# Optimization experiments

Measured on AMD Instinct MI355X. Metric: run time of the kernel, lower is better.

## Reference

```python
import math
import jax, jax.numpy as jnp
import numpy as np

D_MODEL = 1024
L_MAX = 4096
BATCH = 2
FILTER_ORDER = 64
EMB_DIM = 3


def _make_z(L, emb_dim=EMB_DIM):
    # PositionalEmbedding: [time, real bands, imag bands] -> [1, L, emb_dim]
    t = jnp.linspace(0.0, 1.0, L)[None, :, None]
    bands = (emb_dim - 1) // 2
    t_res = jnp.linspace(0.0, L - 1.0, L)[None, :, None]
    w = 2.0 * math.pi * t_res / L
    f = jnp.linspace(1e-4, float(bands - 1), bands)[None, None]
    ph = f * w  # z = exp(-1j*ph) -> real=cos(ph), imag=-sin(ph)
    return jnp.concatenate([t, jnp.cos(ph), -jnp.sin(ph)], axis=-1).astype(jnp.float32)


def setup_inputs() -> dict:
    key = jax.random.key(0)
    ks = jax.random.split(key, 16)
    d = D_MODEL
    iw = 3 * d  # inner_width = d_model * (order + 1), order=2

    def rn(k, shape, scale):
        return (jax.random.normal(k, shape) * scale).astype(jnp.float32)

    return {
        'u': rn(ks[0], (BATCH, L_MAX, d), 1.0),
        'w_in': rn(ks[1], (iw, d), d ** -0.5),
        'b_in': rn(ks[2], (iw,), 0.01),
        'sf_w': rn(ks[3], (iw, 1, 3), 3 ** -0.5),
        'sf_b': rn(ks[4], (iw,), 0.01),
        'z': _make_z(L_MAX),
        'w0': rn(ks[5], (FILTER_ORDER, EMB_DIM), EMB_DIM ** -0.5),
        'b0': rn(ks[6], (FILTER_ORDER,), 0.01),
        'freq': jnp.ones((1, FILTER_ORDER), dtype=jnp.float32),  # Sin(w=1)
        'w1': rn(ks[7], (FILTER_ORDER, FILTER_ORDER), FILTER_ORDER ** -0.5),
        'b1': rn(ks[8], (FILTER_ORDER,), 0.01),
        'w2': rn(ks[9], (FILTER_ORDER, FILTER_ORDER), FILTER_ORDER ** -0.5),
        'b2': rn(ks[10], (FILTER_ORDER,), 0.01),
        'wf': rn(ks[11], (d, FILTER_ORDER), FILTER_ORDER ** -0.5),
        'D': rn(ks[12], (d,), 1.0),
        'w_out': rn(ks[13], (d, d), d ** -0.5),
        'b_out': rn(ks[14], (d,), 0.01),
    }


def _dwconv(x, w, b):
    # depthwise Conv1d(kernel=3, padding=2, groups=C); x: [B, C, L] -> [B, C, L+2]
    y = jax.lax.conv_general_dilated(
        x, w, window_strides=(1,), padding=[(2, 2)],
        feature_group_count=x.shape[1],
        dimension_numbers=('NCH', 'OIH', 'NCH'))
    return y + b[None, :, None]


def _fftconv(v, k, D):
    # circular conv via zero-padded FFT; torch's k_f/fft_size with norm='forward'
    # irfft cancels to the standard (norm='backward') inverse.
    L = v.shape[-1]
    n = 2 * L
    y = jnp.fft.irfft(jnp.fft.rfft(v, n=n) * jnp.fft.rfft(k, n=n), n=n)[..., :L]
    return y + v * D[:, None]


def reference(u, w_in, b_in, sf_w, sf_b, z, w0, b0, freq, w1, b1, w2, b2, wf, D, w_out, b_out):
    b, l, d = u.shape
    L = min(l, L_MAX)

    # input projection + short depthwise filter
    up = jnp.einsum('bld,ed->ble', u, w_in) + b_in  # [b, l, 3d]
    up = up.transpose(0, 2, 1)                       # [b, 3d, l]
    uc = _dwconv(up, sf_w, sf_b)[..., :L]            # [b, 3d, L]
    x0, x1, v = jnp.split(uc, 3, axis=1)             # each [b, d, L]

    # implicit filter MLP with shared Sin activation
    h = jnp.sin(freq * (z @ w0.T + b0))              # [1, L, 64]
    h = jnp.sin(freq * (h @ w1.T + b1))
    h = jnp.sin(freq * (h @ w2.T + b2))
    h = h @ wf.T                                     # [1, L, d]

    # exponential modulation (buffers: t, deltas)
    t = jnp.linspace(0.0, 1.0, L)[None, :, None]
    max_decay = math.log(0.01) / 0.3
    min_decay = math.log(0.01) / 1.5
    deltas = jnp.linspace(min_decay, max_decay, d)[None, None]
    h = h * jnp.exp(-t * jnp.abs(deltas))            # [1, L, d]
    k = h[0].T                                       # [d, L]

    # hyena recurrence (order=2 -> one gated fft conv)
    v = _fftconv(v * x1, k, D)
    y = (v * x0).transpose(0, 2, 1)                  # [b, L, d]
    return jnp.einsum('bld,ed->ble', y, w_out) + b_out
```

## Files before the change

kernel.cpp:

```cpp
#include <hip/hip_runtime.h>
#include <math.h>

#define DM   1024
#define LL   4096
#define NB   2
#define E3   3072
#define FPI  3.14159265358979323846f

typedef __bf16 bf16x8 __attribute__((ext_vector_type(8)));
typedef float  f32x4  __attribute__((ext_vector_type(4)));
typedef _Float16 f16x2 __attribute__((ext_vector_type(2)));

__device__ __forceinline__ unsigned short f2bf(float x) {
    unsigned u = __float_as_uint(x);
    u += 0x7fffu + ((u >> 16) & 1u);
    return (unsigned short)(u >> 16);
}
__device__ __forceinline__ void gload16(void* lds, const void* g) {
    typedef const __attribute__((address_space(1))) unsigned int* gp_t;
    typedef __attribute__((address_space(3))) unsigned int* lp_t;
    __builtin_amdgcn_global_load_lds((gp_t)g, (lp_t)lds, 16, 0, 0);
}

__global__ __launch_bounds__(256) void k_cvt_bf16(
    const float* __restrict__ in, ushort* __restrict__ out, int n4)
{
    int idx = blockIdx.x * 256 + threadIdx.x;
    int stride = gridDim.x * 256;
    for (int i = idx; i < n4; i += stride) {
        float4 v = reinterpret_cast<const float4*>(in)[i];
        ushort4 o;
        o.x = f2bf(v.x); o.y = f2bf(v.y); o.z = f2bf(v.z); o.w = f2bf(v.w);
        *reinterpret_cast<ushort4*>(out + 4 * i) = o;
    }
}

__global__ __launch_bounds__(512, 2) void k_gemm256(
    const ushort* __restrict__ A, const ushort* __restrict__ B,
    const float* __restrict__ bias, float* __restrict__ C,
    int Ntiles, int ldc)
{
    __shared__ __align__(16) char ldsm[131072];
    const int tid  = threadIdx.x;
    const int lane = tid & 63;
    const int w    = tid >> 6;
    const int wr   = w >> 2, wc = w & 3;

    const int cpx = gridDim.x >> 3;
    int swz = (blockIdx.x & 7) * cpx + (blockIdx.x >> 3);
    const int m0 = (swz / Ntiles) << 8;
    const int n0 = (swz % Ntiles) << 8;

    const int r0 = tid >> 2;
    const int swzc = ((tid & 3) ^ ((r0 >> 1) & 3)) << 4;
    const char* Asrc = (const char*)A + ((size_t)(m0 + r0) << 11) + swzc;
    const char* Bsrc = (const char*)B + ((size_t)(n0 + r0) << 11) + swzc;
    char* Ld = ldsm + tid * 16;

    const int lm = lane & 15, lk = lane >> 4;
    const int rA = wr * 128 + lm;
    const int rB = wc * 64 + lm;
    const int aBase = rA * 64 + ((lk ^ ((rA >> 1) & 3)) << 4);
    const int bBase = 32768 + rB * 64 + ((lk ^ ((rB >> 1) & 3)) << 4);

#define STG_A(ks, nb, t1) do { \
    gload16(Ld + (nb) + (ks)*16384,        Asrc + (t1)*128 + (ks)*64); \
    gload16(Ld + (nb) + (ks)*16384 + 8192, Asrc + (t1)*128 + (ks)*64 + 262144); } while(0)
#define STG_B(ks, nb, t1) do { \
    gload16(Ld + (nb) + 32768 + (ks)*16384,        Bsrc + (t1)*128 + (ks)*64); \
    gload16(Ld + (nb) + 32768 + (ks)*16384 + 8192, Bsrc + (t1)*128 + (ks)*64 + 262144); } while(0)
#define LDA(buf, ks, m) (*(const bf16x8*)(ldsm + (buf) + (ks)*16384 + aBase + (m)*1024))
#define LDB(buf, ks, n) (*(const bf16x8*)(ldsm + (buf) + (ks)*16384 + bBase + (n)*1024))
#define VMCNT4() asm volatile("s_waitcnt vmcnt(4)" ::: "memory")
#define VMCNT0() asm volatile("s_waitcnt vmcnt(0)" ::: "memory")
#define BAR() __builtin_amdgcn_s_barrier()

    f32x4 acc[8][4];
#pragma unroll
    for (int i = 0; i < 8; ++i)
#pragma unroll
        for (int j = 0; j < 4; ++j)
#pragma unroll
            for (int r = 0; r < 4; ++r) acc[i][j][r] = 0.f;

    STG_A(0, 0, 0); STG_B(0, 0, 0); STG_A(1, 0, 0); STG_B(1, 0, 0);
    VMCNT4();
    BAR();

    bf16x8 af[4], bq[4];
#pragma unroll 1
    for (int t = 0; t < 15; ++t) {
        const int buf = (t & 1) << 16;
        const int nb  = ((t + 1) & 1) << 16;
        const int t1  = t + 1;
#pragma unroll
        for (int n = 0; n < 4; ++n) bq[n] = LDB(buf, 0, n);
#pragma unroll
        for (int m = 0; m < 4; ++m) af[m] = LDA(buf, 0, m);
        STG_A(0, nb, t1);
        BAR();
        __builtin_amdgcn_s_setprio(1);
#pragma unroll
        for (int m = 0; m < 4; ++m)
#pragma unroll
            for (int n = 0; n < 4; ++n)
                acc[m][n] = __builtin_amdgcn_mfma_f32_16x16x32_bf16(af[m], bq[n], acc[m][n], 0, 0, 0);
        __builtin_amdgcn_s_setprio(0);
        BAR();
#pragma unroll
        for (int m = 0; m < 4; ++m) af[m] = LDA(buf, 0, 4 + m);
        STG_B(0, nb, t1);
        VMCNT4();
        BAR();
        __builtin_amdgcn_s_setprio(1);
#pragma unroll
        for (int m = 0; m < 4; ++m)
#pragma unroll
            for (int n = 0; n < 4; ++n)
                acc[4 + m][n] = __builtin_amdgcn_mfma_f32_16x16x32_bf16(af[m], bq[n], acc[4 + m][n], 0, 0, 0);
        __builtin_amdgcn_s_setprio(0);
        BAR();
#pragma unroll
        for (int n = 0; n < 4; ++n) bq[n] = LDB(buf, 1, n);
#pragma unroll
        for (int m = 0; m < 4; ++m) af[m] = LDA(buf, 1, m);
        STG_A(1, nb, t1);
        BAR();
        __builtin_amdgcn_s_setprio(1);
#pragma unroll
        for (int m = 0; m < 4; ++m)
#pragma unroll
            for (int n = 0; n < 4; ++n)
                acc[m][n] = __builtin_amdgcn_mfma_f32_16x16x32_bf16(af[m], bq[n], acc[m][n], 0, 0, 0);
        __builtin_amdgcn_s_setprio(0);
        BAR();
#pragma unroll
        for (int m = 0; m < 4; ++m) af[m] = LDA(buf, 1, 4 + m);
        STG_B(1, nb, t1);
        VMCNT4();
        BAR();
        __builtin_amdgcn_s_setprio(1);
#pragma unroll
        for (int m = 0; m < 4; ++m)
#pragma unroll
            for (int n = 0; n < 4; ++n)
                acc[4 + m][n] = __builtin_amdgcn_mfma_f32_16x16x32_bf16(af[m], bq[n], acc[4 + m][n], 0, 0, 0);
        __builtin_amdgcn_s_setprio(0);
        BAR();
    }
    {
        const int buf = 1 << 16;
#pragma unroll
        for (int n = 0; n < 4; ++n) bq[n] = LDB(buf, 0, n);
#pragma unroll
        for (int m = 0; m < 4; ++m) af[m] = LDA(buf, 0, m);
        BAR();
#pragma unroll
        for (int m = 0; m < 4; ++m)
#pragma unroll
            for (int n = 0; n < 4; ++n)
                acc[m][n] = __builtin_amdgcn_mfma_f32_16x16x32_bf16(af[m], bq[n], acc[m][n], 0, 0, 0);
        BAR();
#pragma unroll
        for (int m = 0; m < 4; ++m) af[m] = LDA(buf, 0, 4 + m);
        VMCNT0();
        BAR();
#pragma unroll
        for (int m = 0; m < 4; ++m)
#pragma unroll
            for (int n = 0; n < 4; ++n)
                acc[4 + m][n] = __builtin_amdgcn_mfma_f32_16x16x32_bf16(af[m], bq[n], acc[4 + m][n], 0, 0, 0);
        BAR();
#pragma unroll
        for (int n = 0; n < 4; ++n) bq[n] = LDB(buf, 1, n);
#pragma unroll
        for (int m = 0; m < 4; ++m) af[m] = LDA(buf, 1, m);
        BAR();
#pragma unroll
        for (int m = 0; m < 4; ++m)
#pragma unroll
            for (int n = 0; n < 4; ++n)
                acc[m][n] = __builtin_amdgcn_mfma_f32_16x16x32_bf16(af[m], bq[n], acc[m][n], 0, 0, 0);
        BAR();
#pragma unroll
        for (int m = 0; m < 4; ++m) af[m] = LDA(buf, 1, 4 + m);
        BAR();
#pragma unroll
        for (int m = 0; m < 4; ++m)
#pragma unroll
            for (int n = 0; n < 4; ++n)
                acc[4 + m][n] = __builtin_amdgcn_mfma_f32_16x16x32_bf16(af[m], bq[n], acc[4 + m][n], 0, 0, 0);
    }
    const int er = lk << 2, ec = lm;
#pragma unroll
    for (int m = 0; m < 8; ++m) {
        int row = m0 + wr * 128 + m * 16 + er;
#pragma unroll
        for (int n = 0; n < 4; ++n) {
            int col = n0 + wc * 64 + n * 16 + ec;
            float bz = bias[col];
            float* cp = C + (size_t)row * ldc + col;
#pragma unroll
            for (int r = 0; r < 4; ++r)
                cp[(size_t)r * ldc] = acc[m][n][r] + bz;
        }
    }
#undef STG_A
#undef STG_B
#undef LDA
#undef LDB
#undef VMCNT4
#undef VMCNT0
#undef BAR
}

__global__ __launch_bounds__(256) void k_gemm_bf16(
    const ushort* __restrict__ A, const ushort* __restrict__ B,
    const float* __restrict__ bias, float* __restrict__ C, int ldc)
{
    __shared__ ushort As[128 * 32];
    __shared__ ushort Bs[128 * 32];
    const int tid  = threadIdx.x;
    const int lane = tid & 63;
    const int w    = tid >> 6;
    const int wm   = (w >> 1) << 6, wn = (w & 1) << 6;
    const int m0   = blockIdx.y << 7, n0 = blockIdx.x << 7;

    f32x4 acc[4][4];
#pragma unroll
    for (int i = 0; i < 4; ++i)
#pragma unroll
        for (int j = 0; j < 4; ++j)
#pragma unroll
            for (int r = 0; r < 4; ++r) acc[i][j][r] = 0.f;

    const char* Ab = (const char*)A + ((size_t)(m0 + (tid >> 2)) << 11) + ((tid & 3) << 4);
    const char* Bb = (const char*)B + ((size_t)(n0 + (tid >> 2)) << 11) + ((tid & 3) << 4);
    char* AsD = (char*)As + tid * 16;
    char* BsD = (char*)Bs + tid * 16;
    const char* ap = (const char*)As + ((wm + (lane & 15)) << 6) + ((lane >> 4) << 4);
    const char* bp = (const char*)Bs + ((wn + (lane & 15)) << 6) + ((lane >> 4) << 4);

    for (int k0 = 0; k0 < 1024; k0 += 32) {
        __syncthreads();
        gload16(AsD,        Ab + k0 * 2);
        gload16(AsD + 4096, Ab + 131072 + k0 * 2);
        gload16(BsD,        Bb + k0 * 2);
        gload16(BsD + 4096, Bb + 131072 + k0 * 2);
        __syncthreads();
        bf16x8 af[4], bfr[4];
#pragma unroll
        for (int i = 0; i < 4; ++i) {
            af[i]  = *(const bf16x8*)(ap + (i << 10));
            bfr[i] = *(const bf16x8*)(bp + (i << 10));
        }
#pragma unroll
        for (int i = 0; i < 4; ++i)
#pragma unroll
            for (int j = 0; j < 4; ++j)
                acc[i][j] = __builtin_amdgcn_mfma_f32_16x16x32_bf16(
                    af[i], bfr[j], acc[i][j], 0, 0, 0);
    }
    const int er = (lane >> 4) << 2;
    const int ec = lane & 15;
#pragma unroll
    for (int i = 0; i < 4; ++i) {
        int row = m0 + wm + (i << 4) + er;
#pragma unroll
        for (int j = 0; j < 4; ++j) {
            int col = n0 + wn + (j << 4) + ec;
            float bz = bias[col];
            float* cp = C + (size_t)row * ldc + col;
#pragma unroll
            for (int r = 0; r < 4; ++r)
                cp[(size_t)r * ldc] = acc[i][j][r] + bz;
        }
    }
}

__global__ __launch_bounds__(256) void k_dwconv(
    const float* __restrict__ up, const float* __restrict__ sfw,
    const float* __restrict__ sfb, float* __restrict__ x0t,
    float* __restrict__ vin)
{
    __shared__ float xT[32][65];
    __shared__ float vT[32][65];
    const int b  = blockIdx.z;
    const int t0 = blockIdx.y * 64;
    const int c0 = blockIdx.x * 32;
    const int tid = threadIdx.x;
    const int cL = tid & 31, tL = tid >> 5;
    const float* upb = up + (size_t)b * LL * E3;
    const int c = c0 + cL;

#pragma unroll
    for (int r = 0; r < 8; ++r) {
        int t_local = (r << 3) + tL;
        int t = t0 + t_local;
        float res[3];
#pragma unroll
        for (int s3 = 0; s3 < 3; ++s3) {
            int e = c + (s3 << 10);
            float w0 = sfw[e*3+0], w1 = sfw[e*3+1], w2 = sfw[e*3+2];
            float xa = (t >= 2) ? upb[(size_t)(t-2)*E3 + e] : 0.f;
            float xb = (t >= 1) ? upb[(size_t)(t-1)*E3 + e] : 0.f;
            float xc = upb[(size_t)t*E3 + e];
            res[s3] = w0*xa + w1*xb + w2*xc + sfb[e];
        }
        xT[cL][t_local] = res[0];
        vT[cL][t_local] = res[1] * res[2];
    }
    __syncthreads();
    const int cW = tid >> 3, q = tid & 7;
    float tmp[8];
#pragma unroll
    for (int i = 0; i < 8; ++i) tmp[i] = xT[cW][8*q + i];
    size_t off = ((size_t)b * DM + c0 + cW) * LL + t0 + 8*q;
    *reinterpret_cast<float4*>(x0t + off)     = make_float4(tmp[0], tmp[1], tmp[2], tmp[3]);
    *reinterpret_cast<float4*>(x0t + off + 4) = make_float4(tmp[4], tmp[5], tmp[6], tmp[7]);
#pragma unroll
    for (int i = 0; i < 8; ++i) tmp[i] = vT[cW][8*q + i];
    *reinterpret_cast<float4*>(vin + off)     = make_float4(tmp[0], tmp[1], tmp[2], tmp[3]);
    *reinterpret_cast<float4*>(vin + off + 4) = make_float4(tmp[4], tmp[5], tmp[6], tmp[7]);
}

__global__ __launch_bounds__(256) void k_filt_mlp(
    const float* __restrict__ z, const float* __restrict__ w0,
    const float* __restrict__ b0, const float* __restrict__ fr,
    const float* __restrict__ w1, const float* __restrict__ b1,
    const float* __restrict__ w2, const float* __restrict__ b2,
    float* __restrict__ H3)
{
    __shared__ float w1t[64 * 65];
    __shared__ float w2t[64 * 65];
    __shared__ float hb[4][64];
    const int tid = threadIdx.x;
    for (int idx = tid; idx < 4096; idx += 256) {
        int j = idx >> 6, m = idx & 63;
        w1t[m*65 + j] = w1[idx];
        w2t[m*65 + j] = w2[idx];
    }
    __syncthreads();
    const int tl = tid >> 6, j = tid & 63;
    const float frj = fr[j];
    const float b0j = b0[j], b1j = b1[j], b2j = b2[j];
    const float w00 = w0[j*3+0], w01 = w0[j*3+1], w02 = w0[j*3+2];
    const int t0 = blockIdx.x * 64;
    for (int r = 0; r < 16; ++r) {
        int t = t0 + r*4 + tl;
        float z0 = z[t*3+0], z1 = z[t*3+1], z2 = z[t*3+2];
        float h = sinf(frj * (b0j + z0*w00 + z1*w01 + z2*w02));
        hb[tl][j] = h;
        __syncthreads();
        float s = b1j;
#pragma unroll
        for (int m = 0; m < 64; ++m) s = fmaf(hb[tl][m], w1t[m*65 + j], s);
        __syncthreads();
        h = sinf(frj * s);
        hb[tl][j] = h;
        __syncthreads();
        s = b2j;
#pragma unroll
        for (int m = 0; m < 64; ++m) s = fmaf(hb[tl][m], w2t[m*65 + j], s);
        h = sinf(frj * s);
        H3[(size_t)t * 64 + j] = h;
        __syncthreads();
    }
}

__global__ __launch_bounds__(256) void k_filt_k(
    const float* __restrict__ H3, const float* __restrict__ wf,
    float* __restrict__ kf)
{
    __shared__ float Hs[64][65];
    __shared__ float Ws[64][65];
    const int tid = threadIdx.x;
    const int t0 = blockIdx.x * 64, d0 = blockIdx.y * 64;
    for (int idx = tid; idx < 4096; idx += 256) {
        int r = idx >> 6, cc = idx & 63;
        Hs[r][cc] = H3[(size_t)(t0 + r) * 64 + cc];
        Ws[r][cc] = wf[(size_t)(d0 + r) * 64 + cc];
    }
    __syncthreads();
    const int tx = tid & 15, ty = tid >> 4;
    float acc[4][4];
#pragma unroll
    for (int i = 0; i < 4; ++i)
#pragma unroll
        for (int jj = 0; jj < 4; ++jj) acc[i][jj] = 0.f;
#pragma unroll
    for (int j = 0; j < 64; ++j) {
        float wv[4], hv[4];
#pragma unroll
        for (int i = 0; i < 4; ++i) wv[i] = Ws[4*ty + i][j];
#pragma unroll
        for (int i = 0; i < 4; ++i) hv[i] = Hs[4*tx + i][j];
#pragma unroll
        for (int i = 0; i < 4; ++i)
#pragma unroll
            for (int jj = 0; jj < 4; ++jj) acc[i][jj] = fmaf(wv[i], hv[jj], acc[i][jj]);
    }
    const float mind = -3.0701134573253944f;
    const float maxd = -15.350567286626972f;
#pragma unroll
    for (int i = 0; i < 4; ++i) {
        int d = d0 + 4*ty + i;
        float delta = fabsf(mind + (maxd - mind) * ((float)d / 1023.f));
#pragma unroll
        for (int jj = 0; jj < 4; ++jj) {
            int t = t0 + 4*tx + jj;
            float tn = (float)t / 4095.f;
            kf[(size_t)d * LL + t] = acc[i][jj] * expf(-tn * delta);
        }
    }
}

__device__ __forceinline__ int pidx(int p) { return p + (p >> 4); }

__device__ __forceinline__ float2 cmul(float2 a, float2 b) {
    return make_float2(a.x*b.x - a.y*b.y, a.x*b.y + a.y*b.x);
}

__device__ void fft_lds_fwd4(float2* buf, int tid) {
    int lh = 10;
#pragma unroll
    for (int h = 2048; h >= 32; h >>= 2, lh -= 2) {
        const int hh = h >> 1;
        const float rinv = -FPI / (float)h;
        __syncthreads();
#pragma unroll
        for (int r = 0; r < 4; ++r) {
            int bf = (r << 9) + tid;
            int q  = bf & (hh - 1);
            int g  = bf >> lh;
            int j  = (g << (lh + 2)) + q;
            float2 a = buf[pidx(j)];
            float2 b = buf[pidx(j + hh)];
            float2 c = buf[pidx(j + h)];
            float2 d = buf[pidx(j + h + hh)];
            float2 t0 = make_float2(a.x + c.x, a.y + c.y);
            float2 t1 = make_float2(a.x - c.x, a.y - c.y);
            float2 t2 = make_float2(b.x + d.x, b.y + d.y);
            float2 t3 = make_float2(b.y - d.y, d.x - b.x);
            float sn, cs;
            __sincosf(rinv * (float)q, &sn, &cs);
            float c2 = cs*cs - sn*sn, s2 = 2.f*cs*sn;
            float c3 = cs*c2 - sn*s2, s3 = cs*s2 + sn*c2;
            buf[pidx(j)] = make_float2(t0.x + t2.x, t0.y + t2.y);
            float2 e1 = make_float2(t0.x - t2.x, t0.y - t2.y);
            buf[pidx(j + hh)] = make_float2(e1.x*c2 - e1.y*s2, e1.x*s2 + e1.y*c2);
            float2 e2 = make_float2(t1.x + t3.x, t1.y + t3.y);
            buf[pidx(j + h)] = make_float2(e2.x*cs - e2.y*sn, e2.x*sn + e2.y*cs);
            float2 e3 = make_float2(t1.x - t3.x, t1.y - t3.y);
            buf[pidx(j + h + hh)] = make_float2(e3.x*c3 - e3.y*s3, e3.x*s3 + e3.y*c3);
        }
    }
    __syncthreads();
}

__device__ void fft_lds_inv4(float2* buf, int tid) {
    int lh = 4;
#pragma unroll
    for (int h = 32; h <= 2048; h <<= 2, lh += 2) {
        const int hh = h >> 1;
        const float rpos = FPI / (float)h;
        __syncthreads();
#pragma unroll
        for (int r = 0; r < 4; ++r) {
            int bf = (r << 9) + tid;
            int q  = bf & (hh - 1);
            int g  = bf >> lh;
            int j  = (g << (lh + 2)) + q;
            float2 o0 = buf[pidx(j)];
            float2 o1 = buf[pidx(j + hh)];
            float2 o2 = buf[pidx(j + h)];
            float2 o3 = buf[pidx(j + h + hh)];
            float sn, cs;
            __sincosf(rpos * (float)q, &sn, &cs);
            float c2 = cs*cs - sn*sn, s2 = 2.f*cs*sn;
            float c3 = cs*c2 - sn*s2, s3 = cs*s2 + sn*c2;
            float2 p1 = make_float2(o1.x*c2 - o1.y*s2, o1.x*s2 + o1.y*c2);
            float2 p2 = make_float2(o2.x*cs - o2.y*sn, o2.x*sn + o2.y*cs);
            float2 p3 = make_float2(o3.x*c3 - o3.y*s3, o3.x*s3 + o3.y*c3);
            float2 u0 = make_float2(o0.x + p1.x, o0.y + p1.y);
            float2 u1 = make_float2(o0.x - p1.x, o0.y - p1.y);
            float2 u2 = make_float2(p2.x + p3.x, p2.y + p3.y);
            float2 u3 = make_float2(p2.x - p3.x, p2.y - p3.y);
            float2 ib = make_float2(-u3.y, u3.x);
            buf[pidx(j)]          = make_float2(u0.x + u2.x, u0.y + u2.y);
            buf[pidx(j + hh)]     = make_float2(u1.x + ib.x, u1.y + ib.y);
            buf[pidx(j + h)]      = make_float2(u0.x - u2.x, u0.y - u2.y);
            buf[pidx(j + h + hh)] = make_float2(u1.x - ib.x, u1.y - ib.y);
        }
    }
    __syncthreads();
}

__device__ __forceinline__ void fft_reg_fwd(float2* c) {
    const float W16r[8] = {1.f, 0.92387953f, 0.70710678f, 0.38268343f,
                           0.f, -0.38268343f, -0.70710678f, -0.92387953f};
    const float W16i[8] = {0.f, -0.38268343f, -0.70710678f, -0.92387953f,
                           -1.f, -0.92387953f, -0.70710678f, -0.38268343f};
#pragma unroll
    for (int k = 0; k < 8; ++k) {
        float2 a = c[k], b = c[k+8];
        float2 d = make_float2(a.x - b.x, a.y - b.y);
        c[k]   = make_float2(a.x + b.x, a.y + b.y);
        c[k+8] = cmul(d, make_float2(W16r[k], W16i[k]));
    }
    const float W8r[4] = {1.f, 0.70710678f, 0.f, -0.70710678f};
    const float W8i[4] = {0.f, -0.70710678f, -1.f, -0.70710678f};
#pragma unroll
    for (int blk = 0; blk < 16; blk += 8)
#pragma unroll
        for (int k = 0; k < 4; ++k) {
            float2 a = c[blk+k], b = c[blk+k+4];
            float2 d = make_float2(a.x - b.x, a.y - b.y);
            c[blk+k]   = make_float2(a.x + b.x, a.y + b.y);
            c[blk+k+4] = cmul(d, make_float2(W8r[k], W8i[k]));
        }
#pragma unroll
    for (int blk = 0; blk < 16; blk += 4) {
        {   float2 a = c[blk], b = c[blk+2];
            c[blk]   = make_float2(a.x + b.x, a.y + b.y);
            c[blk+2] = make_float2(a.x - b.x, a.y - b.y); }
        {   float2 a = c[blk+1], b = c[blk+3];
            float2 d = make_float2(a.x - b.x, a.y - b.y);
            c[blk+1] = make_float2(a.x + b.x, a.y + b.y);
            c[blk+3] = make_float2(d.y, -d.x); }
    }
#pragma unroll
    for (int blk = 0; blk < 16; blk += 2) {
        float2 a = c[blk], b = c[blk+1];
        c[blk]   = make_float2(a.x + b.x, a.y + b.y);
        c[blk+1] = make_float2(a.x - b.x, a.y - b.y);
    }
}

__device__ __forceinline__ void fft_reg_inv(float2* c) {
#pragma unroll
    for (int blk = 0; blk < 16; blk += 2) {
        float2 a = c[blk], b = c[blk+1];
        c[blk]   = make_float2(a.x + b.x, a.y + b.y);
        c[blk+1] = make_float2(a.x - b.x, a.y - b.y);
    }
#pragma unroll
    for (int blk = 0; blk < 16; blk += 4) {
        {   float2 a = c[blk], b = c[blk+2];
            c[blk]   = make_float2(a.x + b.x, a.y + b.y);
            c[blk+2] = make_float2(a.x - b.x, a.y - b.y); }
        {   float2 a = c[blk+1], b = c[blk+3];
            float2 bt = make_float2(-c[blk+3].y, c[blk+3].x);
            c[blk+1] = make_float2(a.x + bt.x, a.y + bt.y);
            c[blk+3] = make_float2(a.x - bt.x, a.y - bt.y); }
    }
    const float W8r[4] = {1.f, 0.70710678f, 0.f, -0.70710678f};
    const float W8i[4] = {0.f, 0.70710678f, 1.f, 0.70710678f};
#pragma unroll
    for (int blk = 0; blk < 16; blk += 8)
#pragma unroll
        for (int k = 0; k < 4; ++k) {
            float2 a = c[blk+k], b = c[blk+k+4];
            float2 bt = cmul(b, make_float2(W8r[k], W8i[k]));
            c[blk+k]   = make_float2(a.x + bt.x, a.y + bt.y);
            c[blk+k+4] = make_float2(a.x - bt.x, a.y - bt.y);
        }
    const float W16r[8] = {1.f, 0.92387953f, 0.70710678f, 0.38268343f,
                           0.f, -0.38268343f, -0.70710678f, -0.92387953f};
    const float W16i[8] = {0.f, 0.38268343f, 0.70710678f, 0.92387953f,
                           1.f, 0.92387953f, 0.70710678f, 0.38268343f};
#pragma unroll
    for (int k = 0; k < 8; ++k) {
        float2 a = c[k], b = c[k+8];
        float2 bt = cmul(b, make_float2(W16r[k], W16i[k]));
        c[k]   = make_float2(a.x + bt.x, a.y + bt.y);
        c[k+8] = make_float2(a.x - bt.x, a.y - bt.y);
    }
}

__global__ __launch_bounds__(512) void k_kfft(
    const float* __restrict__ kf, f16x2* __restrict__ Kf)
{
    __shared__ float2 buf[8704];
    const int d = blockIdx.x, tid = threadIdx.x;
    const float* krow = kf + (size_t)d * LL;
    const float rinv0 = -FPI / 4096.f;
    for (int i = tid; i < 1024; i += 512) {
        float4 k4 = reinterpret_cast<const float4*>(krow)[i];
        int p = 4 * i;
        float kv[4] = {k4.x, k4.y, k4.z, k4.w};
#pragma unroll
        for (int q = 0; q < 4; ++q) {
            float sn, cs;
            __sincosf(rinv0 * (float)(p + q), &sn, &cs);
            buf[pidx(p + q)]        = make_float2(kv[q], 0.f);
            buf[pidx(p + q + 4096)] = make_float2(kv[q] * cs, kv[q] * sn);
        }
    }
    fft_lds_fwd4(buf, tid);
    float2 c[16];
    const int p0 = tid * 16;
#pragma unroll
    for (int j = 0; j < 16; ++j) c[j] = buf[pidx(p0 + j)];
    fft_reg_fwd(c);
    f16x2* outp = Kf + (size_t)d * 8192 + p0;
#pragma unroll
    for (int j = 0; j < 16; ++j) {
        f16x2 o;
        o[0] = (_Float16)(c[j].x * (1.f/8192.f));
        o[1] = (_Float16)(c[j].y * (1.f/8192.f));
        outp[j] = o;
    }
}

__global__ __launch_bounds__(512) void k_fftconv(
    const float* __restrict__ vin, const f16x2* __restrict__ Kf,
    const float* __restrict__ x0t, const float* __restrict__ Dp,
    ushort* __restrict__ yg)
{
    __shared__ float2 buf[8704];
    const int d = blockIdx.x, tid = threadIdx.x;
    const float* vrow0 = vin + (size_t)d * LL;
    const float* vrow1 = vin + ((size_t)DM + d) * LL;
    const float rinv0 = -FPI / 4096.f;
    for (int i = tid; i < 1024; i += 512) {
        float4 a4 = reinterpret_cast<const float4*>(vrow0)[i];
        float4 b4 = reinterpret_cast<const float4*>(vrow1)[i];
        int p = 4 * i;
        float ar[4] = {a4.x, a4.y, a4.z, a4.w};
        float br[4] = {b4.x, b4.y, b4.z, b4.w};
#pragma unroll
        for (int q = 0; q < 4; ++q) {
            float sn, cs;
            __sincosf(rinv0 * (float)(p + q), &sn, &cs);
            float2 z = make_float2(ar[q], br[q]);
            buf[pidx(p + q)]        = z;
            buf[pidx(p + q + 4096)] = cmul(z, make_float2(cs, sn));
        }
    }
    fft_lds_fwd4(buf, tid);
    float2 c[16];
    const int p0 = tid * 16;
#pragma unroll
    for (int j = 0; j < 16; ++j) c[j] = buf[pidx(p0 + j)];
    fft_reg_fwd(c);
    const f16x2* kfr = Kf + (size_t)d * 8192 + p0;
#pragma unroll
    for (int j = 0; j < 16; ++j) {
        f16x2 kv = kfr[j];
        c[j] = cmul(c[j], make_float2((float)kv[0], (float)kv[1]));
    }
    fft_reg_inv(c);
#pragma unroll
    for (int j = 0; j < 16; ++j) buf[pidx(p0 + j)] = c[j];
    fft_lds_inv4(buf, tid);
    const float Dd = Dp[d];
    const float* xrow0 = x0t + (size_t)d * LL;
    const float* xrow1 = x0t + ((size_t)DM + d) * LL;
    ushort* orow0 = yg + (size_t)d * LL;
    ushort* orow1 = yg + ((size_t)DM + d) * LL;
    const float rinv4 = FPI / 4096.f;
    for (int i = tid; i < 1024; i += 512) {
        float4 v0 = reinterpret_cast<const float4*>(vrow0)[i];
        float4 v1 = reinterpret_cast<const float4*>(vrow1)[i];
        float4 x0 = reinterpret_cast<const float4*>(xrow0)[i];
        float4 x1 = reinterpret_cast<const float4*>(xrow1)[i];
        int p = 4 * i;
        float vr0[4] = {v0.x, v0.y, v0.z, v0.w};
        float vr1[4] = {v1.x, v1.y, v1.z, v1.w};
        float xr0[4] = {x0.x, x0.y, x0.z, x0.w};
        float xr1[4] = {x1.x, x1.y, x1.z, x1.w};
        ushort s0[4], s1[4];
#pragma unroll
        for (int q = 0; q < 4; ++q) {
            float sn, cs;
            __sincosf(rinv4 * (float)(p + q), &sn, &cs);
            float2 a  = buf[pidx(p + q)];
            float2 bb = buf[pidx(p + q + 4096)];
            float2 bt = cmul(bb, make_float2(cs, sn));
            float yre = a.x + bt.x;
            float yim = a.y + bt.y;
            s0[q] = f2bf((yre + Dd * vr0[q]) * xr0[q]);
            s1[q] = f2bf((yim + Dd * vr1[q]) * xr1[q]);
        }
        *reinterpret_cast<ushort4*>(orow0 + p) = make_ushort4(s0[0], s0[1], s0[2], s0[3]);
        *reinterpret_cast<ushort4*>(orow1 + p) = make_ushort4(s1[0], s1[1], s1[2], s1[3]);
    }
}

__global__ __launch_bounds__(256) void k_tr(
    const ushort* __restrict__ yg, ushort* __restrict__ Ag)
{
    __shared__ ushort S[64][72];
    const int b  = blockIdx.z;
    const int d0 = blockIdx.y * 64;
    const int t0 = blockIdx.x * 64;
    const int tid = threadIdx.x;
#pragma unroll
    for (int p = 0; p < 2; ++p) {
        int idx = p * 256 + tid;
        int dr = idx >> 3, c8 = (idx & 7) << 3;
        uint4 v = *reinterpret_cast<const uint4*>(
            yg + ((size_t)b * DM + d0 + dr) * LL + t0 + c8);
        *reinterpret_cast<uint4*>(&S[dr][c8]) = v;
    }
    __syncthreads();
#pragma unroll
    for (int p = 0; p < 2; ++p) {
        int idx = p * 256 + tid;
        int tr = idx >> 3, dq = (idx & 7) << 3;
        ushort tmp[8] __attribute__((aligned(16)));
#pragma unroll
        for (int q = 0; q < 8; ++q) tmp[q] = S[dq + q][tr];
        *reinterpret_cast<uint4*>(Ag + ((size_t)b * LL + t0 + tr) * DM + d0 + dq) =
            *reinterpret_cast<uint4*>(tmp);
    }
}

extern "C" void kernel_launch(void* const* d_in, const int* in_sizes, int n_in,
                              void* d_out, int out_size, void* d_ws, size_t ws_size,
                              hipStream_t stream)
{
    if (n_in < 17) return;
    const float* u    = (const float*)d_in[0];
    const float* w_in = (const float*)d_in[1];
    const float* b_in = (const float*)d_in[2];
    const float* sf_w = (const float*)d_in[3];
    const float* sf_b = (const float*)d_in[4];
    const float* z    = (const float*)d_in[5];
    const float* w0   = (const float*)d_in[6];
    const float* b0   = (const float*)d_in[7];
    const float* freq = (const float*)d_in[8];
    const float* w1   = (const float*)d_in[9];
    const float* b1   = (const float*)d_in[10];
    const float* w2   = (const float*)d_in[11];
    const float* b2   = (const float*)d_in[12];
    const float* wf   = (const float*)d_in[13];
    const float* Dp   = (const float*)d_in[14];
    const float* wout = (const float*)d_in[15];
    const float* bout = (const float*)d_in[16];
    float* out = (float*)d_out;
    float* ws  = (float*)d_ws;

    float*  up    = ws;
    f16x2*  Kf    = (f16x2*)ws;
    float*  kfbuf = ws + 16777216;
    ushort* yg    = (ushort*)(ws + 16777216);
    float*  H3    = ws + 20971520;
    ushort* Ag    = (ushort*)(ws + 20971520);
    ushort* ub    = (ushort*)(ws + 25165824);
    float*  x0t   = ws + 25165824;
    ushort* wb    = (ushort*)(ws + 33554432);
    float*  vin   = ws + 33554432;
    ushort* woutb = (ushort*)(ws + 33554432);
    const size_t NEED = (size_t)41943040 * 4;
    if (ws_size < NEED) return;

    hipLaunchKernelGGL(k_cvt_bf16, dim3(2048), dim3(256), 0, stream, u, ub, 2097152);
    hipLaunchKernelGGL(k_cvt_bf16, dim3(2048), dim3(256), 0, stream, w_in, wb, 786432);
    hipLaunchKernelGGL(k_gemm256, dim3((8192/256) * (E3/256)), dim3(512), 0, stream,
                       ub, wb, b_in, up, E3/256, E3);
    hipLaunchKernelGGL(k_dwconv,   dim3(DM/32, LL/64, NB), dim3(256), 0, stream,
                       up, sf_w, sf_b, x0t, vin);
    hipLaunchKernelGGL(k_filt_mlp, dim3(LL/64), dim3(256), 0, stream,
                       z, w0, b0, freq, w1, b1, w2, b2, H3);
    hipLaunchKernelGGL(k_filt_k,   dim3(LL/64, DM/64), dim3(256), 0, stream,
                       H3, wf, kfbuf);
    hipLaunchKernelGGL(k_kfft,     dim3(DM), dim3(512), 0, stream,
                       kfbuf, Kf);
    hipLaunchKernelGGL(k_fftconv,  dim3(DM), dim3(512), 0, stream,
                       vin, Kf, x0t, Dp, yg);
    hipLaunchKernelGGL(k_cvt_bf16, dim3(1024), dim3(256), 0, stream, wout, woutb, 262144);
    hipLaunchKernelGGL(k_tr,       dim3(LL/64, DM/64, NB), dim3(256), 0, stream,
                       yg, Ag);
    hipLaunchKernelGGL(k_gemm_bf16, dim3(DM/128, 8192/128), dim3(256), 0, stream,
                       Ag, woutb, bout, out, DM);
}
```

Before: 267.5 us.

## Store input projection in bf16, merge conversions, unroll FFT stages, recur twiddles

The input-projection GEMM now writes bf16 instead of fp32, and the depthwise conv widens those values back to float. This halves the traffic on the large intermediate. The two bf16 conversion kernels are merged into one launch. The radix-4 FFT stages are fully unrolled so each stage computes its twiddle once per thread. The pre/post twiddles switch from per-element sincos to a rotation recurrence. The price is bf16 rounding of the projection output and some accumulated twiddle error across four recurrence steps.

```diff
diff --git a/kernel.cpp b/kernel.cpp
--- a/kernel.cpp
+++ b/kernel.cpp
@@ -16,10 +16,31 @@
     u += 0x7fffu + ((u >> 16) & 1u);
     return (unsigned short)(u >> 16);
 }
+__device__ __forceinline__ float bf2f(ushort s) {
+    return __uint_as_float(((unsigned)s) << 16);
+}
 __device__ __forceinline__ void gload16(void* lds, const void* g) {
     typedef const __attribute__((address_space(1))) unsigned int* gp_t;
     typedef __attribute__((address_space(3))) unsigned int* lp_t;
     __builtin_amdgcn_global_load_lds((gp_t)g, (lp_t)lds, 16, 0, 0);
+}
+
+__global__ __launch_bounds__(256) void k_cvt2(
+    const float* __restrict__ a, ushort* __restrict__ oa, int n4a,
+    const float* __restrict__ b, ushort* __restrict__ ob, int n4b)
+{
+    int idx = blockIdx.x * 256 + threadIdx.x;
+    int stride = gridDim.x * 256;
+    int tot = n4a + n4b;
+    for (int i = idx; i < tot; i += stride) {
+        const float4* src; ushort* dst; int k;
+        if (i < n4a) { src = (const float4*)a; dst = oa; k = i; }
+        else         { src = (const float4*)b; dst = ob; k = i - n4a; }
+        float4 v = src[k];
+        ushort4 o;
+        o.x = f2bf(v.x); o.y = f2bf(v.y); o.z = f2bf(v.z); o.w = f2bf(v.w);
+        *reinterpret_cast<ushort4*>(dst + 4 * k) = o;
+    }
 }
 
 __global__ __launch_bounds__(256) void k_cvt_bf16(
@@ -37,7 +58,7 @@
 
 __global__ __launch_bounds__(512, 2) void k_gemm256(
     const ushort* __restrict__ A, const ushort* __restrict__ B,
-    const float* __restrict__ bias, float* __restrict__ C,
+    const float* __restrict__ bias, ushort* __restrict__ C,
     int Ntiles, int ldc)
 {
     __shared__ __align__(16) char ldsm[131072];
@@ -199,10 +220,10 @@
         for (int n = 0; n < 4; ++n) {
             int col = n0 + wc * 64 + n * 16 + ec;
             float bz = bias[col];
-            float* cp = C + (size_t)row * ldc + col;
+            ushort* cp = C + (size_t)row * ldc + col;
 #pragma unroll
             for (int r = 0; r < 4; ++r)
-                cp[(size_t)r * ldc] = acc[m][n][r] + bz;
+                cp[(size_t)r * ldc] = f2bf(acc[m][n][r] + bz);
         }
     }
 #undef STG_A
@@ -279,7 +300,7 @@
 }
 
 __global__ __launch_bounds__(256) void k_dwconv(
-    const float* __restrict__ up, const float* __restrict__ sfw,
+    const ushort* __restrict__ up, const float* __restrict__ sfw,
     const float* __restrict__ sfb, float* __restrict__ x0t,
     float* __restrict__ vin)
 {
@@ -290,7 +311,7 @@
     const int c0 = blockIdx.x * 32;
     const int tid = threadIdx.x;
     const int cL = tid & 31, tL = tid >> 5;
-    const float* upb = up + (size_t)b * LL * E3;
+    const ushort* upb = up + (size_t)b * LL * E3;
     const int c = c0 + cL;
 
 #pragma unroll
@@ -302,9 +323,9 @@
         for (int s3 = 0; s3 < 3; ++s3) {
             int e = c + (s3 << 10);
             float w0 = sfw[e*3+0], w1 = sfw[e*3+1], w2 = sfw[e*3+2];
-            float xa = (t >= 2) ? upb[(size_t)(t-2)*E3 + e] : 0.f;
-            float xb = (t >= 1) ? upb[(size_t)(t-1)*E3 + e] : 0.f;
-            float xc = upb[(size_t)t*E3 + e];
+            float xa = (t >= 2) ? bf2f(upb[(size_t)(t-2)*E3 + e]) : 0.f;
+            float xb = (t >= 1) ? bf2f(upb[(size_t)(t-1)*E3 + e]) : 0.f;
+            float xc = bf2f(upb[(size_t)t*E3 + e]);
             res[s3] = w0*xa + w1*xb + w2*xc + sfb[e];
         }
         xT[cL][t_local] = res[0];
@@ -421,77 +442,153 @@
     return make_float2(a.x*b.x - a.y*b.y, a.x*b.y + a.y*b.x);
 }
 
+__device__ __forceinline__ void r4f_bfly(float2* buf, int j, int hh,
+    float cs, float sn, float c2, float s2, float c3, float s3)
+{
+    float2 a = buf[pidx(j)];
+    float2 b = buf[pidx(j + hh)];
+    float2 c = buf[pidx(j + 2*hh)];
+    float2 d = buf[pidx(j + 3*hh)];
+    float2 t0 = make_float2(a.x + c.x, a.y + c.y);
+    float2 t1 = make_float2(a.x - c.x, a.y - c.y);
+    float2 t2 = make_float2(b.x + d.x, b.y + d.y);
+    float2 t3 = make_float2(b.y - d.y, d.x - b.x);
+    buf[pidx(j)] = make_float2(t0.x + t2.x, t0.y + t2.y);
+    float2 e1 = make_float2(t0.x - t2.x, t0.y - t2.y);
+    buf[pidx(j + hh)]   = make_float2(e1.x*c2 - e1.y*s2, e1.x*s2 + e1.y*c2);
+    float2 e2 = make_float2(t1.x + t3.x, t1.y + t3.y);
+    buf[pidx(j + 2*hh)] = make_float2(e2.x*cs - e2.y*sn, e2.x*sn + e2.y*cs);
+    float2 e3 = make_float2(t1.x - t3.x, t1.y - t3.y);
+    buf[pidx(j + 3*hh)] = make_float2(e3.x*c3 - e3.y*s3, e3.x*s3 + e3.y*c3);
+}
+
+__device__ __forceinline__ void r4i_bfly(float2* buf, int j, int hh,
+    float cs, float sn, float c2, float s2, float c3, float s3)
+{
+    float2 o0 = buf[pidx(j)];
+    float2 o1 = buf[pidx(j + hh)];
+    float2 o2 = buf[pidx(j + 2*hh)];
+    float2 o3 = buf[pidx(j + 3*hh)];
+    float2 p1 = make_float2(o1.x*c2 - o1.y*s2, o1.x*s2 + o1.y*c2);
+    float2 p2 = make_float2(o2.x*cs - o2.y*sn, o2.x*sn + o2.y*cs);
+    float2 p3 = make_float2(o3.x*c3 - o3.y*s3, o3.x*s3 + o3.y*c3);
+    float2 u0 = make_float2(o0.x + p1.x, o0.y + p1.y);
+    float2 u1 = make_float2(o0.x - p1.x, o0.y - p1.y);
+    float2 u2 = make_float2(p2.x + p3.x, p2.y + p3.y);
+    float2 u3 = make_float2(p2.x - p3.x, p2.y - p3.y);
+    float2 ib = make_float2(-u3.y, u3.x);
+    buf[pidx(j)]        = make_float2(u0.x + u2.x, u0.y + u2.y);
+    buf[pidx(j + hh)]   = make_float2(u1.x + ib.x, u1.y + ib.y);
+    buf[pidx(j + 2*hh)] = make_float2(u0.x - u2.x, u0.y - u2.y);
+    buf[pidx(j + 3*hh)] = make_float2(u1.x - ib.x, u1.y - ib.y);
+}
+
+#define TWCHAIN(cs, sn, c2, s2, c3, s3) \
+    float c2 = cs*cs - sn*sn, s2 = 2.f*cs*sn; \
+    float c3 = cs*c2 - sn*s2, s3 = cs*s2 + sn*c2
+
 __device__ void fft_lds_fwd4(float2* buf, int tid) {
-    int lh = 10;
-#pragma unroll
-    for (int h = 2048; h >= 32; h >>= 2, lh -= 2) {
-        const int hh = h >> 1;
-        const float rinv = -FPI / (float)h;
-        __syncthreads();
-#pragma unroll
-        for (int r = 0; r < 4; ++r) {
-            int bf = (r << 9) + tid;
-            int q  = bf & (hh - 1);
-            int g  = bf >> lh;
-            int j  = (g << (lh + 2)) + q;
-            float2 a = buf[pidx(j)];
-            float2 b = buf[pidx(j + hh)];
-            float2 c = buf[pidx(j + h)];
-            float2 d = buf[pidx(j + h + hh)];
-            float2 t0 = make_float2(a.x + c.x, a.y + c.y);
-            float2 t1 = make_float2(a.x - c.x, a.y - c.y);
-            float2 t2 = make_float2(b.x + d.x, b.y + d.y);
-            float2 t3 = make_float2(b.y - d.y, d.x - b.x);
-            float sn, cs;
-            __sincosf(rinv * (float)q, &sn, &cs);
-            float c2 = cs*cs - sn*sn, s2 = 2.f*cs*sn;
-            float c3 = cs*c2 - sn*s2, s3 = cs*s2 + sn*c2;
-            buf[pidx(j)] = make_float2(t0.x + t2.x, t0.y + t2.y);
-            float2 e1 = make_float2(t0.x - t2.x, t0.y - t2.y);
-            buf[pidx(j + hh)] = make_float2(e1.x*c2 - e1.y*s2, e1.x*s2 + e1.y*c2);
-            float2 e2 = make_float2(t1.x + t3.x, t1.y + t3.y);
-            buf[pidx(j + h)] = make_float2(e2.x*cs - e2.y*sn, e2.x*sn + e2.y*cs);
-            float2 e3 = make_float2(t1.x - t3.x, t1.y - t3.y);
-            buf[pidx(j + h + hh)] = make_float2(e3.x*c3 - e3.y*s3, e3.x*s3 + e3.y*c3);
-        }
+    {
+        const float rinv = -FPI / 2048.f;
+        float sna, csa; __sincosf(rinv * (float)tid, &sna, &csa);
+        const float KC = 0.70710678118654752f, KS = -0.70710678118654752f;
+        float csb = csa*KC - sna*KS, snb = csa*KS + sna*KC;
+        TWCHAIN(csa, sna, c2a, s2a, c3a, s3a);
+        TWCHAIN(csb, snb, c2b, s2b, c3b, s3b);
+        __syncthreads();
+        r4f_bfly(buf, tid,        1024, csa, sna, c2a, s2a, c3a, s3a);
+        r4f_bfly(buf, tid + 512,  1024, csb, snb, c2b, s2b, c3b, s3b);
+        r4f_bfly(buf, tid + 4096, 1024, csa, sna, c2a, s2a, c3a, s3a);
+        r4f_bfly(buf, tid + 4608, 1024, csb, snb, c2b, s2b, c3b, s3b);
+    }
+    {
+        const float rinv = -FPI / 512.f;
+        int q = tid & 255;
+        float sn, cs; __sincosf(rinv * (float)q, &sn, &cs);
+        TWCHAIN(cs, sn, c2, s2, c3, s3);
+        int jb = ((tid >> 8) << 10) + q;
+        __syncthreads();
+        r4f_bfly(buf, jb,        256, cs, sn, c2, s2, c3, s3);
+        r4f_bfly(buf, jb + 2048, 256, cs, sn, c2, s2, c3, s3);
+        r4f_bfly(buf, jb + 4096, 256, cs, sn, c2, s2, c3, s3);
+        r4f_bfly(buf, jb + 6144, 256, cs, sn, c2, s2, c3, s3);
+    }
+    {
+        const float rinv = -FPI / 128.f;
+        int q = tid & 63;
+        float sn, cs; __sincosf(rinv * (float)q, &sn, &cs);
+        TWCHAIN(cs, sn, c2, s2, c3, s3);
+        int jb = ((tid >> 6) << 8) + q;
+        __syncthreads();
+        r4f_bfly(buf, jb,        64, cs, sn, c2, s2, c3, s3);
+        r4f_bfly(buf, jb + 2048, 64, cs, sn, c2, s2, c3, s3);
+        r4f_bfly(buf, jb + 4096, 64, cs, sn, c2, s2, c3, s3);
+        r4f_bfly(buf, jb + 6144, 64, cs, sn, c2, s2, c3, s3);
+    }
+    {
+        const float rinv = -FPI / 32.f;
+        int q = tid & 15;
+        float sn, cs; __sincosf(rinv * (float)q, &sn, &cs);
+        TWCHAIN(cs, sn, c2, s2, c3, s3);
+        int jb = ((tid >> 4) << 6) + q;
+        __syncthreads();
+        r4f_bfly(buf, jb,        16, cs, sn, c2, s2, c3, s3);
+        r4f_bfly(buf, jb + 2048, 16, cs, sn, c2, s2, c3, s3);
+        r4f_bfly(buf, jb + 4096, 16, cs, sn, c2, s2, c3, s3);
+        r4f_bfly(buf, jb + 6144, 16, cs, sn, c2, s2, c3, s3);
     }
     __syncthreads();
 }
 
 __device__ void fft_lds_inv4(float2* buf, int tid) {
-    int lh = 4;
-#pragma unroll
-    for (int h = 32; h <= 2048; h <<= 2, lh += 2) {
-        const int hh = h >> 1;
-        const float rpos = FPI / (float)h;
-        __syncthreads();
-#pragma unroll
-        for (int r = 0; r < 4; ++r) {
-            int bf = (r << 9) + tid;
-            int q  = bf & (hh - 1);
-            int g  = bf >> lh;
-            int j  = (g << (lh + 2)) + q;
-            float2 o0 = buf[pidx(j)];
-            float2 o1 = buf[pidx(j + hh)];
-            float2 o2 = buf[pidx(j + h)];
-            float2 o3 = buf[pidx(j + h + hh)];
-            float sn, cs;
-            __sincosf(rpos * (float)q, &sn, &cs);
-            float c2 = cs*cs - sn*sn, s2 = 2.f*cs*sn;
-            float c3 = cs*c2 - sn*s2, s3 = cs*s2 + sn*c2;
-            float2 p1 = make_float2(o1.x*c2 - o1.y*s2, o1.x*s2 + o1.y*c2);
-            float2 p2 = make_float2(o2.x*cs - o2.y*sn, o2.x*sn + o2.y*cs);
-            float2 p3 = make_float2(o3.x*c3 - o3.y*s3, o3.x*s3 + o3.y*c3);
-            float2 u0 = make_float2(o0.x + p1.x, o0.y + p1.y);
-            float2 u1 = make_float2(o0.x - p1.x, o0.y - p1.y);
-            float2 u2 = make_float2(p2.x + p3.x, p2.y + p3.y);
-            float2 u3 = make_float2(p2.x - p3.x, p2.y - p3.y);
-            float2 ib = make_float2(-u3.y, u3.x);
-            buf[pidx(j)]          = make_float2(u0.x + u2.x, u0.y + u2.y);
-            buf[pidx(j + hh)]     = make_float2(u1.x + ib.x, u1.y + ib.y);
-            buf[pidx(j + h)]      = make_float2(u0.x - u2.x, u0.y - u2.y);
-            buf[pidx(j + h + hh)] = make_float2(u1.x - ib.x, u1.y - ib.y);
-        }
+    {
+        const float rpos = FPI / 32.f;
+        int q = tid & 15;
+        float sn, cs; __sincosf(rpos * (float)q, &sn, &cs);
+        TWCHAIN(cs, sn, c2, s2, c3, s3);
+        int jb = ((tid >> 4) << 6) + q;
+        __syncthreads();
+        r4i_bfly(buf, jb,        16, cs, sn, c2, s2, c3, s3);
+        r4i_bfly(buf, jb + 2048, 16, cs, sn, c2, s2, c3, s3);
+        r4i_bfly(buf, jb + 4096, 16, cs, sn, c2, s2, c3, s3);
+        r4i_bfly(buf, jb + 6144, 16, cs, sn, c2, s2, c3, s3);
+    }
+    {
+        const float rpos = FPI / 128.f;
+        int q = tid & 63;
+        float sn, cs; __sincosf(rpos * (float)q, &sn, &cs);
+        TWCHAIN(cs, sn, c2, s2, c3, s3);
+        int jb = ((tid >> 6) << 8) + q;
+        __syncthreads();
+        r4i_bfly(buf, jb,        64, cs, sn, c2, s2, c3, s3);
+        r4i_bfly(buf, jb + 2048, 64, cs, sn, c2, s2, c3, s3);
+        r4i_bfly(buf, jb + 4096, 64, cs, sn, c2, s2, c3, s3);
+        r4i_bfly(buf, jb + 6144, 64, cs, sn, c2, s2, c3, s3);
+    }
+    {
+        const float rpos = FPI / 512.f;
+        int q = tid & 255;
+        float sn, cs; __sincosf(rpos * (float)q, &sn, &cs);
+        TWCHAIN(cs, sn, c2, s2, c3, s3);
+        int jb = ((tid >> 8) << 10) + q;
+        __syncthreads();
+        r4i_bfly(buf, jb,        256, cs, sn, c2, s2, c3, s3);
+        r4i_bfly(buf, jb + 2048, 256, cs, sn, c2, s2, c3, s3);
+        r4i_bfly(buf, jb + 4096, 256, cs, sn, c2, s2, c3, s3);
+        r4i_bfly(buf, jb + 6144, 256, cs, sn, c2, s2, c3, s3);
+    }
+    {
+        const float rpos = FPI / 2048.f;
+        float sna, csa; __sincosf(rpos * (float)tid, &sna, &csa);
+        const float KC = 0.70710678118654752f, KS = 0.70710678118654752f;
+        float csb = csa*KC - sna*KS, snb = csa*KS + sna*KC;
+        TWCHAIN(csa, sna, c2a, s2a, c3a, s3a);
+        TWCHAIN(csb, snb, c2b, s2b, c3b, s3b);
+        __syncthreads();
+        r4i_bfly(buf, tid,        1024, csa, sna, c2a, s2a, c3a, s3a);
+        r4i_bfly(buf, tid + 512,  1024, csb, snb, c2b, s2b, c3b, s3b);
+        r4i_bfly(buf, tid + 4096, 1024, csa, sna, c2a, s2a, c3a, s3a);
+        r4i_bfly(buf, tid + 4608, 1024, csb, snb, c2b, s2b, c3b, s3b);
     }
     __syncthreads();
 }
@@ -578,6 +675,9 @@
     }
 }
 
+#define RC4096 0.99999970586288222f
+#define RS4096 7.66990318742704e-4f
+
 __global__ __launch_bounds__(512) void k_kfft(
     const float* __restrict__ kf, f16x2* __restrict__ Kf)
 {
@@ -589,12 +689,15 @@
         float4 k4 = reinterpret_cast<const float4*>(krow)[i];
         int p = 4 * i;
         float kv[4] = {k4.x, k4.y, k4.z, k4.w};
+        float sn, cs;
+        __sincosf(rinv0 * (float)p, &sn, &cs);
 #pragma unroll
         for (int q = 0; q < 4; ++q) {
-            float sn, cs;
-            __sincosf(rinv0 * (float)(p + q), &sn, &cs);
             buf[pidx(p + q)]        = make_float2(kv[q], 0.f);
             buf[pidx(p + q + 4096)] = make_float2(kv[q] * cs, kv[q] * sn);
+            float nc = cs * RC4096 + sn * RS4096;
+            float ns = sn * RC4096 - cs * RS4096;
+            cs = nc; sn = ns;
         }
     }
     fft_lds_fwd4(buf, tid);
@@ -629,13 +732,16 @@
         int p = 4 * i;
         float ar[4] = {a4.x, a4.y, a4.z, a4.w};
         float br[4] = {b4.x, b4.y, b4.z, b4.w};
+        float sn, cs;
+        __sincosf(rinv0 * (float)p, &sn, &cs);
 #pragma unroll
         for (int q = 0; q < 4; ++q) {
-            float sn, cs;
-            __sincosf(rinv0 * (float)(p + q), &sn, &cs);
             float2 z = make_float2(ar[q], br[q]);
             buf[pidx(p + q)]        = z;
             buf[pidx(p + q + 4096)] = cmul(z, make_float2(cs, sn));
+            float nc = cs * RC4096 + sn * RS4096;
+            float ns = sn * RC4096 - cs * RS4096;
+            cs = nc; sn = ns;
         }
     }
     fft_lds_fwd4(buf, tid);
@@ -671,10 +777,10 @@
         float xr0[4] = {x0.x, x0.y, x0.z, x0.w};
         float xr1[4] = {x1.x, x1.y, x1.z, x1.w};
         ushort s0[4], s1[4];
+        float sn, cs;
+        __sincosf(rinv4 * (float)p, &sn, &cs);
 #pragma unroll
         for (int q = 0; q < 4; ++q) {
-            float sn, cs;
-            __sincosf(rinv4 * (float)(p + q), &sn, &cs);
             float2 a  = buf[pidx(p + q)];
             float2 bb = buf[pidx(p + q + 4096)];
             float2 bt = cmul(bb, make_float2(cs, sn));
@@ -682,6 +788,9 @@
             float yim = a.y + bt.y;
             s0[q] = f2bf((yre + Dd * vr0[q]) * xr0[q]);
             s1[q] = f2bf((yim + Dd * vr1[q]) * xr1[q]);
+            float nc = cs * RC4096 - sn * RS4096;
+            float ns = sn * RC4096 + cs * RS4096;
+            cs = nc; sn = ns;
         }
         *reinterpret_cast<ushort4*>(orow0 + p) = make_ushort4(s0[0], s0[1], s0[2], s0[3]);
         *reinterpret_cast<ushort4*>(orow1 + p) = make_ushort4(s1[0], s1[1], s1[2], s1[3]);
@@ -742,7 +851,7 @@
     float* out = (float*)d_out;
     float* ws  = (float*)d_ws;
 
-    float*  up    = ws;
+    ushort* up    = (ushort*)ws;
     f16x2*  Kf    = (f16x2*)ws;
     float*  kfbuf = ws + 16777216;
     ushort* yg    = (ushort*)(ws + 16777216);
@@ -756,9 +865,9 @@
     const size_t NEED = (size_t)41943040 * 4;
     if (ws_size < NEED) return;
 
-    hipLaunchKernelGGL(k_cvt_bf16, dim3(2048), dim3(256), 0, stream, u, ub, 2097152);
-    hipLaunchKernelGGL(k_cvt_bf16, dim3(2048), dim3(256), 0, stream, w_in, wb, 786432);
-    hipLaunchKernelGGL(k_gemm256, dim3((8192/256) * (E3/256)), dim3(512), 0, stream,
+    hipLaunchKernelGGL(k_cvt2,     dim3(2048), dim3(256), 0, stream,
+                       u, ub, 2097152, w_in, wb, 786432);
+    hipLaunchKernelGGL(k_gemm256,  dim3((8192/256) * (E3/256)), dim3(512), 0, stream,
                        ub, wb, b_in, up, E3/256, E3);
     hipLaunchKernelGGL(k_dwconv,   dim3(DM/32, LL/64, NB), dim3(256), 0, stream,
                        up, sf_w, sf_b, x0t, vin);
```

After: 277.9 us. 1.04x slower.
